# Performance work log

Hardware: AMD Instinct MI355X
Metric: run time of the kernel (lower is better)

Reference implementation:

```python
import jax, jax.numpy as jnp
import numpy as np
from jax import lax

RADIUS = 4
SIGMA_1 = 5.0
SIGMA_2 = 1.0


def _gaussian_kernel_3d(radius, sigma):
    x = np.linspace(-radius, radius, 2 * radius + 1)
    xx, yy, zz = np.meshgrid(x, x, x)
    dist2 = xx ** 2 + yy ** 2 + zz ** 2
    k = np.exp(-dist2 / (2.0 * sigma ** 2)).astype(np.float32)
    return jnp.asarray(k)[None, None]  # [O=1, I=1, D, H, W]


def _conv3d_same(x, kernel, radius):
    # x: [B,1,D,H,W], kernel: [1,1,kd,kh,kw]
    pad = [(radius, radius)] * 3
    return lax.conv_general_dilated(
        x, kernel, window_strides=(1, 1, 1), padding=pad,
        dimension_numbers=('NCDHW', 'OIDHW', 'NCDHW'))


def setup_inputs() -> dict:
    key = jax.random.key(0)
    k1, k2 = jax.random.split(key)
    labels = jax.random.uniform(k1, (4, 1, 160, 160, 160), dtype=jnp.float32)
    inputs = jax.random.uniform(k2, (4, 1, 160, 160, 160), dtype=jnp.float32)
    return {"labels": labels, "inputs": inputs}


def reference(labels, inputs):
    kernel = _gaussian_kernel_3d(RADIUS, SIGMA_1)
    num_classes = 2
    p0 = labels[:, 0:1]  # [B,1,D,H,W]
    loss = jnp.float32(0.0)
    for k in range(num_classes):
        class_probs = p0 if k == 0 else 1.0 - p0
        class_mean = (jnp.mean(inputs * class_probs, axis=(2, 3, 4), keepdims=True)
                      / (jnp.mean(class_probs, axis=(2, 3, 4), keepdims=True) + 1e-5))
        diff = jnp.sum((inputs - class_mean) ** 2, axis=1, keepdims=True)  # [B,1,D,H,W]
        weights = jnp.exp(-(diff ** 2) / (SIGMA_2 ** 2))
        numerator = jnp.sum(class_probs * _conv3d_same(class_probs * weights, kernel, RADIUS))
        denominator = jnp.sum(class_probs * _conv3d_same(weights, kernel, RADIUS))
        # L1Loss(scalar, 0) == abs(scalar)
        loss = loss + jnp.abs(numerator / (denominator + 1e-6))
    return jnp.float32(num_classes) - loss
```

## Files before the change

### kernel.cpp

```cpp
#include <hip/hip_runtime.h>
#include <hip/hip_fp16.h>
#include <math.h>

#define NX   160
#define N2   25600
#define N3   4096000
#define NB   4

#define YCH  10
#define NBLK_XY 1600
#define XY_BLKS_PER_B 400

#define ZCH  10
#define NBLK_Z 1600

__device__ inline int xcd_swz(int bid, int nblk) {
    return (bid & 7) * (nblk >> 3) + (bid >> 3);
}

__device__ __constant__ float G1[9] = {
    0.72614903f, 0.83527021f, 0.92311635f, 0.98019867f, 1.0f,
    0.98019867f, 0.92311635f, 0.83527021f, 0.72614903f};

#define ES_FULL 7.92946852f
__device__ __constant__ float ES_M[4] = {3.46473426f, 2.48453559f, 1.56141924f,
                                         0.72614903f};
__device__ inline float edge_sum(int i) {
    float s = ES_FULL;
    if (i < 4) s -= ES_M[i];
    if (i > NX - 5) s -= ES_M[NX - 1 - i];
    return s;
}

__device__ inline float4 f4_zero() { return make_float4(0.f, 0.f, 0.f, 0.f); }
__device__ inline float4 f4_axpy(float a, float4 b, float4 c) {
    return make_float4(c.x + a * b.x, c.y + a * b.y, c.z + a * b.z, c.w + a * b.w);
}

__device__ inline float4 load_t4(const __half* p) {
    uint2 u = *(const uint2*)p;
    __half2 a = *(const __half2*)&u.x;
    __half2 b = *(const __half2*)&u.y;
    float2 fa = __half22float2(a);
    float2 fb = __half22float2(b);
    return make_float4(fa.x, fa.y, fb.x, fb.y);
}

template <int NV>
__device__ inline void block_reduce_store(double* vals, double* dst) {
    __shared__ double red[4][NV];
    int lane = threadIdx.x & 63;
    int wave = threadIdx.x >> 6;
#pragma unroll
    for (int v = 0; v < NV; ++v) {
        double x = vals[v];
#pragma unroll
        for (int off = 32; off > 0; off >>= 1) x += __shfl_down(x, off, 64);
        if (lane == 0) red[wave][v] = x;
    }
    __syncthreads();
    if (threadIdx.x < NV) {
        int v = threadIdx.x;
        dst[v] = red[0][v] + red[1][v] + red[2][v] + red[3][v];
    }
}

__global__ __launch_bounds__(256) void conv_xy_kernel(
    const float* __restrict__ labels, const float* __restrict__ inputs,
    __half* __restrict__ t, double* __restrict__ pS) {
    int tid = threadIdx.x;
    int lbid = xcd_swz(blockIdx.x, NBLK_XY);
    int tidg = lbid * 256 + tid;
    int x4 = tidg % 40;
    int r = tidg / 40;
    int yc = r % 16;
    r /= 16;
    int z = r % NX;
    int b = r / NX;

    int x0 = x4 * 4;
    int y0 = yc * YCH;
    const float* plane = labels + b * N3 + z * N2;
    const float* iplane = inputs + b * N3 + z * N2;
    __half* tplane = t + b * N3 + z * N2;

    float4 win[9];
#pragma unroll
    for (int d = 0; d < 9; ++d) {
        int gy = y0 - 4 + d;
        bool rowok = (gy >= 0) && (gy < NX);
        float w[12];
#pragma unroll
        for (int c = 0; c < 3; ++c) {
            int gx = x0 - 4 + 4 * c;
            float4 v = (rowok && gx >= 0 && gx <= NX - 4)
                           ? *(const float4*)&plane[gy * NX + gx]
                           : f4_zero();
            w[4 * c] = v.x; w[4 * c + 1] = v.y;
            w[4 * c + 2] = v.z; w[4 * c + 3] = v.w;
        }
        float4 o = f4_zero();
#pragma unroll
        for (int k = 0; k < 9; ++k) {
            float g = G1[k];
            o.x += g * w[k];     o.y += g * w[k + 1];
            o.z += g * w[k + 2]; o.w += g * w[k + 3];
        }
        win[d] = o;
    }

    double sp = 0.0, sip = 0.0, si = 0.0;
#pragma unroll 2
    for (int yo = 0; yo < YCH; ++yo) {
        int y = y0 + yo;
        int gy = y + 5;
        bool rowok = (gy < NX) && (yo < YCH - 1);
        float w[12];
#pragma unroll
        for (int c = 0; c < 3; ++c) {
            int gx = x0 - 4 + 4 * c;
            float4 v = (rowok && gx >= 0 && gx <= NX - 4)
                           ? *(const float4*)&plane[gy * NX + gx]
                           : f4_zero();
            w[4 * c] = v.x; w[4 * c + 1] = v.y;
            w[4 * c + 2] = v.z; w[4 * c + 3] = v.w;
        }
        int go = y * NX + x0;
        float4 p = *(const float4*)&plane[go];
        float4 in = *(const float4*)&iplane[go];
        float4 acc = f4_zero();
#pragma unroll
        for (int d = 0; d < 9; ++d) acc = f4_axpy(G1[d], win[d], acc);
        __half2 ha = __floats2half2_rn(acc.x, acc.y);
        __half2 hb = __floats2half2_rn(acc.z, acc.w);
        uint2 u;
        u.x = *(unsigned int*)&ha;
        u.y = *(unsigned int*)&hb;
        *(uint2*)&tplane[go] = u;
        sp += (double)(p.x + p.y + p.z + p.w);
        sip += (double)(in.x * p.x + in.y * p.y + in.z * p.z + in.w * p.w);
        si += (double)(in.x + in.y + in.z + in.w);
        float4 o = f4_zero();
#pragma unroll
        for (int k = 0; k < 9; ++k) {
            float g = G1[k];
            o.x += g * w[k];     o.y += g * w[k + 1];
            o.z += g * w[k + 2]; o.w += g * w[k + 3];
        }
#pragma unroll
        for (int d = 0; d < 8; ++d) win[d] = win[d + 1];
        win[8] = o;
    }
    double vals[3] = {sp, sip, si};
    block_reduce_store<3>(vals, pS + 3 * lbid);
}

__global__ __launch_bounds__(256) void conv_z_kernel(
    const __half* __restrict__ t, const float* __restrict__ labels,
    const float* __restrict__ inputs, const double* __restrict__ pS,
    double* __restrict__ pZ) {
    int tid = threadIdx.x;
    int lbid = xcd_swz(blockIdx.x, NBLK_Z);
    int tidg = lbid * 256 + tid;
    int x4 = tidg % 40;
    int r = tidg / 40;
    int y = r % NX;
    r /= NX;
    int zc = r % 16;
    int b = r / 16;

    __shared__ float sM[2];
    {
        double v0 = 0, v1 = 0, v2 = 0;
        for (int i = tid; i < XY_BLKS_PER_B; i += 256) {
            const double* p = pS + 3 * (b * XY_BLKS_PER_B + i);
            v0 += p[0]; v1 += p[1]; v2 += p[2];
        }
        __shared__ double red[4][3];
        int lane = tid & 63, wave = tid >> 6;
        double vals[3] = {v0, v1, v2};
#pragma unroll
        for (int v = 0; v < 3; ++v) {
            double x = vals[v];
#pragma unroll
            for (int off = 32; off > 0; off >>= 1) x += __shfl_down(x, off, 64);
            if (lane == 0) red[wave][v] = x;
        }
        __syncthreads();
        if (tid == 0) {
            double sp = red[0][0] + red[1][0] + red[2][0] + red[3][0];
            double sip = red[0][1] + red[1][1] + red[2][1] + red[3][1];
            double si = red[0][2] + red[1][2] + red[2][2] + red[3][2];
            const double Nv = (double)N3;
            sM[0] = (float)((sip / Nv) / (sp / Nv + 1e-5));
            sM[1] = (float)(((si - sip) / Nv) / ((Nv - sp) / Nv + 1e-5));
        }
        __syncthreads();
    }
    float m0 = sM[0], m1 = sM[1];

    int x = x4 * 4;
    float ey = edge_sum(y);
    float cx[4] = {edge_sum(x) * ey, edge_sum(x + 1) * ey,
                   edge_sum(x + 2) * ey, edge_sum(x + 3) * ey};

    int z0 = zc * ZCH;
    int base = b * N3 + y * NX + x;

    float4 win[9];
#pragma unroll
    for (int d = 0; d < 9; ++d) {
        int z = z0 - 4 + d;
        win[d] = (z >= 0 && z < NX) ? load_t4(&t[base + z * N2]) : f4_zero();
    }

    float n0 = 0.f, d0 = 0.f, n1 = 0.f, d1 = 0.f;
    for (int zb = 0; zb < 5; ++zb) {
        int z = z0 + 2 * zb;
        float4 tn[2], pv[2], iv[2];
#pragma unroll
        for (int j = 0; j < 2; ++j) {
            int zl = z + j + 5;
            tn[j] = (zl < NX) ? load_t4(&t[base + zl * N2]) : f4_zero();
            int gi = base + (z + j) * N2;
            pv[j] = *(const float4*)&labels[gi];
            iv[j] = *(const float4*)&inputs[gi];
        }
#pragma unroll
        for (int j = 0; j < 2; ++j) {
            float4 c4 = f4_zero();
#pragma unroll
            for (int d = 0; d < 9; ++d) c4 = f4_axpy(G1[d], win[d], c4);
            float ez = edge_sum(z + j);
            float pc[4] = {pv[j].x, pv[j].y, pv[j].z, pv[j].w};
            float ic[4] = {iv[j].x, iv[j].y, iv[j].z, iv[j].w};
            float cc[4] = {c4.x, c4.y, c4.z, c4.w};
#pragma unroll
            for (int l = 0; l < 4; ++l) {
                float c1 = cx[l] * ez - cc[l];
                float df0 = ic[l] - m0; df0 *= df0;
                float w0 = __expf(-df0 * df0);
                float df1 = ic[l] - m1; df1 *= df1;
                float w1 = __expf(-df1 * df1);
                n0 += cc[l] * pc[l] * w0;
                d0 += cc[l] * w0;
                n1 += c1 * (1.f - pc[l]) * w1;
                d1 += c1 * w1;
            }
#pragma unroll
            for (int d = 0; d < 8; ++d) win[d] = win[d + 1];
            win[8] = tn[j];
        }
    }
    double vals[4] = {(double)n0, (double)d0, (double)n1, (double)d1};
    block_reduce_store<4>(vals, pZ + 4 * lbid);
}

__global__ __launch_bounds__(256) void finalize_kernel(
    const double* __restrict__ pZ, float* __restrict__ out) {
    double a0 = 0, a1 = 0, a2 = 0, a3 = 0;
    for (int i = threadIdx.x; i < NBLK_Z; i += 256) {
        const double* p = &pZ[4 * i];
        a0 += p[0]; a1 += p[1]; a2 += p[2]; a3 += p[3];
    }
    __shared__ double red[4][4];
    int lane = threadIdx.x & 63;
    int wave = threadIdx.x >> 6;
    double vals[4] = {a0, a1, a2, a3};
#pragma unroll
    for (int v = 0; v < 4; ++v) {
        double x = vals[v];
#pragma unroll
        for (int off = 32; off > 0; off >>= 1) x += __shfl_down(x, off, 64);
        if (lane == 0) red[wave][v] = x;
    }
    __syncthreads();
    if (threadIdx.x == 0) {
        double acc[4];
#pragma unroll
        for (int v = 0; v < 4; ++v)
            acc[v] = red[0][v] + red[1][v] + red[2][v] + red[3][v];
        double r0 = fabs(acc[0] / (acc[1] + 1e-6));
        double r1 = fabs(acc[2] / (acc[3] + 1e-6));
        out[0] = (float)(2.0 - r0 - r1);
    }
}

extern "C" void kernel_launch(void* const* d_in, const int* in_sizes, int n_in,
                              void* d_out, int out_size, void* d_ws, size_t ws_size,
                              hipStream_t stream) {
    const float* labels = (const float*)d_in[0];
    const float* inputs = (const float*)d_in[1];
    float* out = (float*)d_out;

    double* pS = (double*)d_ws;
    double* pZ = (double*)((char*)d_ws + 192128);
    __half* t  = (__half*)((char*)d_ws + 524288);

    hipLaunchKernelGGL(conv_xy_kernel, dim3(NBLK_XY), dim3(256), 0, stream,
                       labels, inputs, t, pS);
    hipLaunchKernelGGL(conv_z_kernel, dim3(NBLK_Z), dim3(256), 0, stream,
                       t, labels, inputs, pS, pZ);
    hipLaunchKernelGGL(finalize_kernel, dim3(1), dim3(256), 0, stream, pZ, out);
}
```

Before: 201.4 us.

## Map z-slabs to XCDs and double the z-chunk per thread in conv_z

Both kernels now assign each of the 8 XCDs a contiguous 20-plane z-slab, using blockIdx&7 as the XCD id. The blurred intermediate t written by the xy pass is then mostly re-read by the z pass on the same XCD, which should improve L2 hit rates. The z pass also processes 20 z-planes per thread instead of 10, with 4-plane batches of loads, so the 8-plane halo is reloaded less often. In exchange it launches half as many z-pass blocks, which lowers parallelism and raises register pressure per thread.

```diff
diff --git a/kernel.cpp b/kernel.cpp
--- a/kernel.cpp
+++ b/kernel.cpp
@@ -9,14 +9,10 @@
 
 #define YCH  10
 #define NBLK_XY 1600
-#define XY_BLKS_PER_B 400
-
-#define ZCH  10
-#define NBLK_Z 1600
-
-__device__ inline int xcd_swz(int bid, int nblk) {
-    return (bid & 7) * (nblk >> 3) + (bid >> 3);
-}
+#define ZSLAB 20
+
+#define ZCH  20
+#define NBLK_Z 800
 
 __device__ __constant__ float G1[9] = {
     0.72614903f, 0.83527021f, 0.92311635f, 0.98019867f, 1.0f,
@@ -69,14 +65,15 @@
     const float* __restrict__ labels, const float* __restrict__ inputs,
     __half* __restrict__ t, double* __restrict__ pS) {
     int tid = threadIdx.x;
-    int lbid = xcd_swz(blockIdx.x, NBLK_XY);
-    int tidg = lbid * 256 + tid;
-    int x4 = tidg % 40;
-    int r = tidg / 40;
-    int yc = r % 16;
-    r /= 16;
-    int z = r % NX;
-    int b = r / NX;
+    int xcd = blockIdx.x & 7;
+    int v   = blockIdx.x >> 3;
+    int idx = v * 256 + tid;
+    int x4  = idx % 40;
+    int rest = idx / 40;
+    int yc  = rest % 16;
+    int zb  = rest / 16;
+    int z   = (zb % ZSLAB) + ZSLAB * xcd;
+    int b   = zb / ZSLAB;
 
     int x0 = x4 * 4;
     int y0 = yc * YCH;
@@ -93,11 +90,11 @@
 #pragma unroll
         for (int c = 0; c < 3; ++c) {
             int gx = x0 - 4 + 4 * c;
-            float4 v = (rowok && gx >= 0 && gx <= NX - 4)
-                           ? *(const float4*)&plane[gy * NX + gx]
-                           : f4_zero();
-            w[4 * c] = v.x; w[4 * c + 1] = v.y;
-            w[4 * c + 2] = v.z; w[4 * c + 3] = v.w;
+            float4 vv = (rowok && gx >= 0 && gx <= NX - 4)
+                            ? *(const float4*)&plane[gy * NX + gx]
+                            : f4_zero();
+            w[4 * c] = vv.x; w[4 * c + 1] = vv.y;
+            w[4 * c + 2] = vv.z; w[4 * c + 3] = vv.w;
         }
         float4 o = f4_zero();
 #pragma unroll
@@ -119,11 +116,11 @@
 #pragma unroll
         for (int c = 0; c < 3; ++c) {
             int gx = x0 - 4 + 4 * c;
-            float4 v = (rowok && gx >= 0 && gx <= NX - 4)
-                           ? *(const float4*)&plane[gy * NX + gx]
-                           : f4_zero();
-            w[4 * c] = v.x; w[4 * c + 1] = v.y;
-            w[4 * c + 2] = v.z; w[4 * c + 3] = v.w;
+            float4 vv = (rowok && gx >= 0 && gx <= NX - 4)
+                            ? *(const float4*)&plane[gy * NX + gx]
+                            : f4_zero();
+            w[4 * c] = vv.x; w[4 * c + 1] = vv.y;
+            w[4 * c + 2] = vv.z; w[4 * c + 3] = vv.w;
         }
         int go = y * NX + x0;
         float4 p = *(const float4*)&plane[go];
@@ -152,7 +149,7 @@
         win[8] = o;
     }
     double vals[3] = {sp, sip, si};
-    block_reduce_store<3>(vals, pS + 3 * lbid);
+    block_reduce_store<3>(vals, pS + 3 * blockIdx.x);
 }
 
 __global__ __launch_bounds__(256) void conv_z_kernel(
@@ -160,20 +157,20 @@
     const float* __restrict__ inputs, const double* __restrict__ pS,
     double* __restrict__ pZ) {
     int tid = threadIdx.x;
-    int lbid = xcd_swz(blockIdx.x, NBLK_Z);
-    int tidg = lbid * 256 + tid;
-    int x4 = tidg % 40;
-    int r = tidg / 40;
-    int y = r % NX;
-    r /= NX;
-    int zc = r % 16;
-    int b = r / 16;
+    int xcd = blockIdx.x & 7;
+    int c   = blockIdx.x >> 3;
+    int idx = c * 256 + tid;
+    int x4 = idx % 40;
+    int rest = idx / 40;
+    int y = rest % NX;
+    int b = rest / NX;
+    int z0 = ZSLAB * xcd;
 
     __shared__ float sM[2];
     {
         double v0 = 0, v1 = 0, v2 = 0;
-        for (int i = tid; i < XY_BLKS_PER_B; i += 256) {
-            const double* p = pS + 3 * (b * XY_BLKS_PER_B + i);
+        for (int i = tid; i < 400; i += 256) {
+            const double* p = pS + 3 * (400 * b + i);
             v0 += p[0]; v1 += p[1]; v2 += p[2];
         }
         __shared__ double red[4][3];
@@ -204,7 +201,6 @@
     float cx[4] = {edge_sum(x) * ey, edge_sum(x + 1) * ey,
                    edge_sum(x + 2) * ey, edge_sum(x + 3) * ey};
 
-    int z0 = zc * ZCH;
     int base = b * N3 + y * NX + x;
 
     float4 win[9];
@@ -215,11 +211,11 @@
     }
 
     float n0 = 0.f, d0 = 0.f, n1 = 0.f, d1 = 0.f;
-    for (int zb = 0; zb < 5; ++zb) {
-        int z = z0 + 2 * zb;
-        float4 tn[2], pv[2], iv[2];
-#pragma unroll
-        for (int j = 0; j < 2; ++j) {
+    for (int zb5 = 0; zb5 < 5; ++zb5) {
+        int z = z0 + 4 * zb5;
+        float4 tn[4], pv[4], iv[4];
+#pragma unroll
+        for (int j = 0; j < 4; ++j) {
             int zl = z + j + 5;
             tn[j] = (zl < NX) ? load_t4(&t[base + zl * N2]) : f4_zero();
             int gi = base + (z + j) * N2;
@@ -227,7 +223,7 @@
             iv[j] = *(const float4*)&inputs[gi];
         }
 #pragma unroll
-        for (int j = 0; j < 2; ++j) {
+        for (int j = 0; j < 4; ++j) {
             float4 c4 = f4_zero();
 #pragma unroll
             for (int d = 0; d < 9; ++d) c4 = f4_axpy(G1[d], win[d], c4);
@@ -253,7 +249,7 @@
         }
     }
     double vals[4] = {(double)n0, (double)d0, (double)n1, (double)d1};
-    block_reduce_store<4>(vals, pZ + 4 * lbid);
+    block_reduce_store<4>(vals, pZ + 4 * blockIdx.x);
 }
 
 __global__ __launch_bounds__(256) void finalize_kernel(
```

New measurement: 196.5 us. 1.03x faster.
